# Kernel tuning notes

Hardware: AMD Instinct MI355X
Metric: run time of the kernel (lower is better)

## Reference

```python
import jax, jax.numpy as jnp
import numpy as np

T, D, F, E, K = 2048, 512, 2048, 8, 2


def setup_inputs() -> dict:
    key = jax.random.key(0)
    ks = jax.random.split(key, 5)
    scaled = lambda k, shape, fan: jax.random.normal(k, shape, jnp.float32) * (fan ** -0.5)
    x = jax.random.normal(ks[0], (T, D), jnp.float32)
    Wg = scaled(ks[1], (D, E), D)          # gate: Linear(D -> E), no bias
    W1 = scaled(ks[2], (E, D, F), D)       # per-expert up proj
    W3 = scaled(ks[3], (E, D, F), D)       # per-expert gate proj (SwiGLU)
    W2 = scaled(ks[4], (E, F, D), F)       # per-expert down proj
    return {"x": x, "Wg": Wg, "W1": W1, "W2": W2, "W3": W3}


def reference(x, Wg, W1, W2, W3):
    # gate logits + top-k routing (topk over raw logits, softmax over the k picked logits,
    # computed in float32 then cast back -- matches the torch source)
    logits = x @ Wg                                   # [T, E]
    topw, sel = jax.lax.top_k(logits, K)              # [T, K] each
    weights = jax.nn.softmax(topw.astype(jnp.float32), axis=-1).astype(x.dtype)
    out = jnp.zeros_like(x)
    # NOTE: the source uses `output[batch_idx] = ...` (assignment, not +=), so later
    # experts OVERWRITE earlier ones for tokens routed to multiple experts.
    # We replicate that exactly with sequential jnp.where overwrites.
    for i in range(E):
        hit = sel == i                                # [T, K]
        mask = hit.any(axis=-1)                       # [T] tokens routed to expert i
        w_i = jnp.sum(jnp.where(hit, weights, 0.0), axis=-1)  # [T] routing weight
        h = jax.nn.silu(x @ W1[i]) * (x @ W3[i])      # [T, F] SwiGLU
        y = h @ W2[i]                                 # [T, D]
        out = jnp.where(mask[:, None], w_i[:, None] * y, out)
    return out
```

## Files before the change

kernel.cpp:

```cpp
#include <hip/hip_runtime.h>
#include <hip/hip_bf16.h>
#include <math.h>

typedef __attribute__((ext_vector_type(8))) short short8;
typedef __attribute__((ext_vector_type(4))) float f32x4;

#define T_TOK 2048
#define D_DIM 512
#define F_DIM 2048
#define E_NUM 8
#define MAXT1 40

__device__ __forceinline__ unsigned short f2bf(float f) {
  union { float f; unsigned u; } c; c.f = f;
  unsigned u = c.u;
  return (unsigned short)((u + 0x7fffu + ((u >> 16) & 1u)) >> 16);
}

__device__ __forceinline__ void gld16(const void* g, void* l) {
  __builtin_amdgcn_global_load_lds((const __attribute__((address_space(1))) int*)g,
                                   (__attribute__((address_space(3))) int*)l, 16, 0, 0);
}

__global__ __launch_bounds__(256) void k_route(const float* __restrict__ xin,
                                               const float* __restrict__ Wg,
                                               int* __restrict__ jbuf,
                                               float* __restrict__ wbuf,
                                               unsigned short* __restrict__ xb) {
  int gid = blockIdx.x * 256 + threadIdx.x;
  int t = gid >> 5, seg = gid & 31;
  const float* xp = xin + (size_t)t * D_DIM + seg * 16;
  unsigned short* xo = xb + (size_t)t * D_DIM + seg * 16;
  float acc[8];
#pragma unroll
  for (int e = 0; e < 8; ++e) acc[e] = 0.f;
#pragma unroll
  for (int i = 0; i < 4; ++i) {
    float4 v = *(const float4*)(xp + i * 4);
    ushort4 o;
    o.x = f2bf(v.x); o.y = f2bf(v.y); o.z = f2bf(v.z); o.w = f2bf(v.w);
    *(ushort4*)(xo + i * 4) = o;
    const float* xs = (const float*)&v;
#pragma unroll
    for (int q = 0; q < 4; ++q) {
      int d = seg * 16 + i * 4 + q;
      const float4* wr = (const float4*)(Wg + (size_t)d * 8);
      float4 w0 = wr[0], w1 = wr[1];
      acc[0] += xs[q] * w0.x; acc[1] += xs[q] * w0.y;
      acc[2] += xs[q] * w0.z; acc[3] += xs[q] * w0.w;
      acc[4] += xs[q] * w1.x; acc[5] += xs[q] * w1.y;
      acc[6] += xs[q] * w1.z; acc[7] += xs[q] * w1.w;
    }
  }
#pragma unroll
  for (int off = 1; off < 32; off <<= 1)
#pragma unroll
    for (int e = 0; e < 8; ++e) acc[e] += __shfl_xor(acc[e], off);
  if (seg == 0) {
    float l0 = -1e30f, l1 = -1e30f; int i0 = 0, i1 = 0;
#pragma unroll
    for (int e = 0; e < 8; ++e) {
      float l = acc[e];
      if (l > l0) { l1 = l0; i1 = i0; l0 = l; i0 = e; }
      else if (l > l1) { l1 = l; i1 = e; }
    }
    int j; float w;
    if (i0 > i1) { j = i0; w = 1.f / (1.f + expf(l1 - l0)); }
    else         { j = i1; w = 1.f / (1.f + expf(l0 - l1)); }
    jbuf[t] = j; wbuf[t] = w;
  }
}

__global__ __launch_bounds__(256) void k_prep2(const float* __restrict__ W1,
                                               const float* __restrict__ W3,
                                               unsigned short* __restrict__ w1f,
                                               unsigned short* __restrict__ w3f,
                                               const int* __restrict__ jbuf,
                                               int* __restrict__ cntp,
                                               int* __restrict__ basep,
                                               int* __restrict__ list,
                                               int* __restrict__ tl1,
                                               int* __restrict__ ntl) {
  __shared__ float4 tile4[2][64 * 32];
  __shared__ int scnt[8], scur[8];
  int bz = blockIdx.x, tid = threadIdx.x;

  if (bz >= 1024) {
    if (tid < 8) scnt[tid] = 0;
    __syncthreads();
    for (int t = tid; t < T_TOK; t += 256) atomicAdd(&scnt[jbuf[t]], 1);
    __syncthreads();
    if (tid == 0) {
      int run = 0;
      for (int e = 0; e < 8; ++e) {
        cntp[e] = scnt[e]; basep[e] = run; scur[e] = run;
        run += scnt[e];
      }
      int n1 = 0, bb = 0;
      for (int e = 0; e < 8; ++e) {
        for (int m = 0; m < scnt[e]; m += 64) tl1[n1++] = (e << 16) | (bb + m);
        bb += scnt[e];
      }
      ntl[0] = n1;
    }
    __syncthreads();
    for (int t = tid; t < T_TOK; t += 256) {
      int j = jbuf[t];
      int p = atomicAdd(&scur[j], 1);
      list[p] = t;
    }
    return;
  }

  int z = bz >> 6, rem = bz & 63;
  const int K = 512, N = 2048;
  int n0 = (rem & 15) * 128, k0 = (rem >> 4) * 128;
  size_t zsz = (size_t)(K / 32) * (N / 16) * 512;
  const float* in; unsigned short* out;
  if (z < 8) { in = W1 + (size_t)z * K * N;       out = w1f + (size_t)z * zsz; }
  else       { in = W3 + (size_t)(z - 8) * K * N; out = w3f + (size_t)(z - 8) * zsz; }

  int lr = tid >> 5, lc = tid & 31;
  int wv = tid >> 6, l = tid & 63;
  int n4l = (l & 15) >> 2, nr = l & 3, kg = (l >> 4) * 8;

  auto loadT = [&](int buf, int kb0) {
#pragma unroll
    for (int it = 0; it < 8; ++it) {
      int row = it * 8 + lr;
      float4 v = *(const float4*)(in + (size_t)(kb0 + row) * N + n0 + lc * 4);
      tile4[buf][row * 32 + ((lc + (row >> 3) * 4) & 31)] = v;
    }
  };
  auto storeT = [&](int buf, int kb0) {
    const float* tf = (const float*)&tile4[buf][0];
#pragma unroll
    for (int q = 0; q < 4; ++q) {
      int fid = wv * 4 + q;
      int nb = fid >> 1, kb = fid & 1;
      int n4 = nb * 4 + n4l;
      short8 o;
#pragma unroll
      for (int j = 0; j < 8; ++j) {
        int k = kb * 32 + kg + j;
        int slot = k * 32 + ((n4 + (k >> 3) * 4) & 31);
        o[j] = (short)f2bf(tf[slot * 4 + nr]);
      }
      unsigned short* op = out + (((size_t)(n0 / 16 + nb) * (K / 32)) + (kb0 / 32 + kb)) * 512 + l * 8;
      *(short8*)op = o;
    }
  };

  loadT(0, k0);
  __syncthreads();
  loadT(1, k0 + 64);
  storeT(0, k0);
  __syncthreads();
  storeT(1, k0 + 64);
}

__global__ __launch_bounds__(256, 2) void k_ffn1w2(const unsigned short* __restrict__ xb,
                                                   const unsigned short* __restrict__ w1f,
                                                   const unsigned short* __restrict__ w3f,
                                                   const float* __restrict__ W2,
                                                   unsigned short* __restrict__ w2f,
                                                   const int* __restrict__ cntp,
                                                   const int* __restrict__ basep,
                                                   const int* __restrict__ list,
                                                   const int* __restrict__ tl1,
                                                   const int* __restrict__ ntl,
                                                   unsigned short* __restrict__ hbuf) {
  __shared__ __align__(16) unsigned short sA[64 * 512];
  int tid = threadIdx.x, wv = tid >> 6, l = tid & 63;

  if (blockIdx.x >= 640) {
    int idx = blockIdx.x - 640;
    int z = idx >> 6, rem = idx & 63;
    const int K = 2048, N = 512;
    int n0 = (rem & 3) * 128, k0 = (rem >> 2) * 128;
    size_t zsz = (size_t)(K / 32) * (N / 16) * 512;
    const float* in = W2 + (size_t)z * K * N;
    unsigned short* out = w2f + (size_t)z * zsz;
    float4* tile4 = (float4*)sA;

    int lr = tid >> 5, lc = tid & 31;
    int n4l = (l & 15) >> 2, nr = l & 3, kg = (l >> 4) * 8;

    auto loadT = [&](int buf, int kb0) {
#pragma unroll
      for (int it = 0; it < 8; ++it) {
        int row = it * 8 + lr;
        float4 v = *(const float4*)(in + (size_t)(kb0 + row) * N + n0 + lc * 4);
        tile4[buf * 2048 + row * 32 + ((lc + (row >> 3) * 4) & 31)] = v;
      }
    };
    auto storeT = [&](int buf, int kb0) {
      const float* tf = (const float*)&tile4[buf * 2048];
#pragma unroll
      for (int q = 0; q < 4; ++q) {
        int fid = wv * 4 + q;
        int nb = fid >> 1, kb = fid & 1;
        int n4 = nb * 4 + n4l;
        short8 o;
#pragma unroll
        for (int j = 0; j < 8; ++j) {
          int k = kb * 32 + kg + j;
          int slot = k * 32 + ((n4 + (k >> 3) * 4) & 31);
          o[j] = (short)f2bf(tf[slot * 4 + nr]);
        }
        unsigned short* op = out + (((size_t)(n0 / 16 + nb) * (K / 32)) + (kb0 / 32 + kb)) * 512 + l * 8;
        *(short8*)op = o;
      }
    };

    loadT(0, k0);
    __syncthreads();
    loadT(1, k0 + 64);
    storeT(0, k0);
    __syncthreads();
    storeT(1, k0 + 64);
    return;
  }

  int L = blockIdx.x;
  int b = (L & 7) * 80 + (L >> 3);
  int x = b % 40, y = b / 40;
  if (x >= ntl[0]) return;
  int pk = tl1[x];
  int e = pk >> 16, g0 = pk & 0xffff;
  int lim = basep[e] + cntp[e];
  int wr = wv >> 1, wc = wv & 1;

#pragma unroll
  for (int it = 0; it < 16; ++it) {
    int row = wv * 16 + it;
    int gr = g0 + row; if (gr >= lim) gr = lim - 1;
    int tok = list[gr];
    int slot = (l & 56) | ((l & 7) ^ (row & 7));
    gld16(xb + (size_t)tok * D_DIM + slot * 8, sA + row * 512);
  }

  const unsigned short* w1b = w1f + ((size_t)(e * 128 + y * 8 + wc) * 16) * 512 + l * 8;
  const unsigned short* w3b = w3f + ((size_t)(e * 128 + y * 8 + wc) * 16) * 512 + l * 8;

  short8 P1[8], P3[8], Q1[8], Q3[8];
  auto loadS = [&](short8* r1, short8* r3, int s) {
    int g = s >> 1, h = s & 1;
    const unsigned short* p1 = w1b + ((size_t)(g * 32 + h * 8)) * 512;
    const unsigned short* p3 = w3b + ((size_t)(g * 32 + h * 8)) * 512;
#pragma unroll
    for (int q = 0; q < 8; ++q) {
      r1[q] = *(const short8*)(p1 + (size_t)q * 512);
      r3[q] = *(const short8*)(p3 + (size_t)q * 512);
    }
  };

  f32x4 au[2], av[2];
  auto halfC = [&](const short8* r1, const short8* r3, int h) {
#pragma unroll
    for (int q = 0; q < 8; ++q) {
      int kf = h * 8 + q;
      short8 a[2];
#pragma unroll
      for (int i = 0; i < 2; ++i) {
        int r = wr * 32 + i * 16 + (l & 15);
        int slot = kf * 4 + (l >> 4);
        int swz = (slot & 56) | ((slot & 7) ^ (r & 7));
        a[i] = *(const short8*)(sA + r * 512 + swz * 8);
      }
#pragma unroll
      for (int i = 0; i < 2; ++i) {
        au[i] = __builtin_amdgcn_mfma_f32_16x16x32_bf16(a[i], r1[q], au[i], 0, 0, 0);
        av[i] = __builtin_amdgcn_mfma_f32_16x16x32_bf16(a[i], r3[q], av[i], 0, 0, 0);
      }
    }
  };

  loadS(P1, P3, 0);
  __syncthreads();

  int cloc = l & 15, rb = (l >> 4) * 4;
#pragma unroll
  for (int gp = 0; gp < 4; ++gp) {
#pragma unroll
    for (int i = 0; i < 2; ++i) {
      au[i] = (f32x4){0.f, 0.f, 0.f, 0.f};
      av[i] = (f32x4){0.f, 0.f, 0.f, 0.f};
    }
    loadS(Q1, Q3, gp * 2 + 1);
    halfC(P1, P3, 0);
    if (gp < 3) loadS(P1, P3, gp * 2 + 2);
    halfC(Q1, Q3, 1);
    int col = (y * 4 + gp) * 32 + wc * 16 + cloc;
#pragma unroll
    for (int i = 0; i < 2; ++i)
#pragma unroll
      for (int r = 0; r < 4; ++r) {
        int gr = g0 + wr * 32 + i * 16 + rb + r;
        if (gr < lim) {
          float uu = au[i][r], vv = av[i][r];
          float hh = (uu / (1.f + expf(-uu))) * vv;
          hbuf[(size_t)gr * F_DIM + col] = f2bf(hh);
        }
      }
  }
}

__global__ __launch_bounds__(256, 3) void k_ffn2(const unsigned short* __restrict__ hbuf,
                                                 const unsigned short* __restrict__ w2f,
                                                 const int* __restrict__ cntp,
                                                 const int* __restrict__ basep,
                                                 const int* __restrict__ list,
                                                 const int* __restrict__ tl1,
                                                 const int* __restrict__ ntl,
                                                 const float* __restrict__ wbuf,
                                                 float* __restrict__ out) {
  int L = blockIdx.x;
  int c = L & 7, q = L >> 3;
  int x = c * 5 + (q % 5);
  int nt = q / 5;
  if (x >= ntl[0]) return;
  int pk = tl1[x];
  int e = pk >> 16, g0 = pk & 0xffff;
  int lim = basep[e] + cntp[e];
  __shared__ unsigned short sA[2 * 8192];
  int tid = threadIdx.x, wv = tid >> 6, l = tid & 63;
  int wr = wv >> 1, wc = wv & 1;

  auto stage = [&](int buf, int ck) {
#pragma unroll
    for (int it = 0; it < 4; ++it) {
      int row0 = it * 16 + wv * 4;
      int row = row0 + (l >> 4);
      int gr = g0 + row; if (gr > T_TOK - 1) gr = T_TOK - 1;
      int sl = (l & 8) | ((l & 7) ^ (row & 7));
      gld16(hbuf + (size_t)gr * F_DIM + ck * 128 + sl * 8, sA + buf * 8192 + row0 * 128);
    }
  };

  const unsigned short* b2p = w2f + ((size_t)(e * 32 + nt * 2 + wc) * 64) * 512 + l * 8;

  short8 Ba[4], Bb[4];
  auto loadB = [&](short8* B, int ck) {
#pragma unroll
    for (int kk = 0; kk < 4; ++kk)
      B[kk] = *(const short8*)(b2p + (size_t)(ck * 4 + kk) * 512);
  };

  f32x4 acc[2];
  acc[0] = (f32x4){0.f, 0.f, 0.f, 0.f};
  acc[1] = (f32x4){0.f, 0.f, 0.f, 0.f};

  auto compute = [&](const short8* B, int cur) {
#pragma unroll
    for (int kk = 0; kk < 4; ++kk) {
      short8 a[2];
#pragma unroll
      for (int i = 0; i < 2; ++i) {
        int r = wr * 32 + i * 16 + (l & 15);
        int slot = kk * 4 + (l >> 4);
        int swz = (slot & 8) | ((slot & 7) ^ (r & 7));
        a[i] = *(const short8*)(sA + cur * 8192 + r * 128 + swz * 8);
      }
      acc[0] = __builtin_amdgcn_mfma_f32_16x16x32_bf16(a[0], B[kk], acc[0], 0, 0, 0);
      acc[1] = __builtin_amdgcn_mfma_f32_16x16x32_bf16(a[1], B[kk], acc[1], 0, 0, 0);
    }
  };

  stage(0, 0);
  loadB(Ba, 0);
  __syncthreads();
  int cur = 0;
  for (int ck = 0; ck < 16; ck += 2) {
    stage(cur ^ 1, ck + 1);
    loadB(Bb, ck + 1);
    compute(Ba, cur);
    __syncthreads();
    cur ^= 1;
    if (ck + 2 < 16) {
      stage(cur ^ 1, ck + 2);
      loadB(Ba, ck + 2);
    }
    compute(Bb, cur);
    __syncthreads();
    cur ^= 1;
  }

  int cloc = l & 15, rb = (l >> 4) * 4;
#pragma unroll
  for (int i = 0; i < 2; ++i)
#pragma unroll
    for (int r = 0; r < 4; ++r) {
      int gr = g0 + wr * 32 + i * 16 + rb + r;
      if (gr < lim) {
        int tok = list[gr];
        out[(size_t)tok * D_DIM + nt * 32 + wc * 16 + cloc] = wbuf[tok] * acc[i][r];
      }
    }
}

extern "C" void kernel_launch(void* const* d_in, const int* in_sizes, int n_in,
                              void* d_out, int out_size, void* d_ws, size_t ws_size,
                              hipStream_t stream) {
  const float* x  = (const float*)d_in[0];
  const float* Wg = (const float*)d_in[1];
  const float* W1 = (const float*)d_in[2];
  const float* W2 = (const float*)d_in[3];
  const float* W3 = (const float*)d_in[4];
  float* out = (float*)d_out;
  char* ws = (char*)d_ws;

  int*            jbuf  = (int*)(ws + 0);
  float*          wbuf  = (float*)(ws + 8192);
  int*            cntp  = (int*)(ws + 16384);
  int*            basep = (int*)(ws + 16448);
  int*            list  = (int*)(ws + 16640);
  int*            tl1   = (int*)(ws + 24832);
  int*            ntl   = (int*)(ws + 25600);
  unsigned short* xb    = (unsigned short*)(ws + 32768);
  unsigned short* w1f   = (unsigned short*)(ws + 32768 + 2097152);
  unsigned short* w3f   = (unsigned short*)(ws + 32768 + 2097152 + 16777216);
  unsigned short* w2f   = (unsigned short*)(ws + 32768 + 2097152 + 2 * 16777216);
  unsigned short* hbuf  = (unsigned short*)(ws + 32768 + 2097152 + 3 * 16777216);

  k_route<<<dim3(256), dim3(256), 0, stream>>>(x, Wg, jbuf, wbuf, xb);
  k_prep2<<<dim3(1025), dim3(256), 0, stream>>>(W1, W3, w1f, w3f, jbuf, cntp, basep, list, tl1, ntl);
  k_ffn1w2<<<dim3(1152), dim3(256), 0, stream>>>(xb, w1f, w3f, W2, w2f, cntp, basep, list, tl1, ntl, hbuf);
  k_ffn2<<<dim3(640), dim3(256), 0, stream>>>(hbuf, w2f, cntp, basep, list, tl1, ntl, wbuf, out);
}
```

Before: 80.19 us.

## Shrink FFN1 column tile to 64 per block and double the block count

Each FFN1 block now computes 64 rows by 64 F-columns instead of 64 by 128. The four waves split the columns, and each wave covers all 64 rows with four MFMA accumulator tiles. This doubles the number of FFN1 blocks (the grid goes from 1152 to 1792), so parallelism is higher and per-block latency is shorter. In exchange, each 64x512 token tile is staged into LDS twice as often, and every block still pays the full x-gather cost for half as much compute.

```diff
diff --git a/kernel.cpp b/kernel.cpp
--- a/kernel.cpp
+++ b/kernel.cpp
@@ -173,8 +173,8 @@
   __shared__ __align__(16) unsigned short sA[64 * 512];
   int tid = threadIdx.x, wv = tid >> 6, l = tid & 63;
 
-  if (blockIdx.x >= 640) {
-    int idx = blockIdx.x - 640;
+  if (blockIdx.x >= 1280) {
+    int idx = blockIdx.x - 1280;
     int z = idx >> 6, rem = idx & 63;
     const int K = 2048, N = 512;
     int n0 = (rem & 3) * 128, k0 = (rem >> 2) * 128;
@@ -223,13 +223,12 @@
   }
 
   int L = blockIdx.x;
-  int b = (L & 7) * 80 + (L >> 3);
+  int b = (L & 7) * 160 + (L >> 3);
   int x = b % 40, y = b / 40;
   if (x >= ntl[0]) return;
   int pk = tl1[x];
   int e = pk >> 16, g0 = pk & 0xffff;
   int lim = basep[e] + cntp[e];
-  int wr = wv >> 1, wc = wv & 1;
 
 #pragma unroll
   for (int it = 0; it < 16; ++it) {
@@ -240,36 +239,39 @@
     gld16(xb + (size_t)tok * D_DIM + slot * 8, sA + row * 512);
   }
 
-  const unsigned short* w1b = w1f + ((size_t)(e * 128 + y * 8 + wc) * 16) * 512 + l * 8;
-  const unsigned short* w3b = w3f + ((size_t)(e * 128 + y * 8 + wc) * 16) * 512 + l * 8;
-
-  short8 P1[8], P3[8], Q1[8], Q3[8];
+  const unsigned short* w1b = w1f + ((size_t)(e * 128 + y * 4 + wv) * 16) * 512 + l * 8;
+  const unsigned short* w3b = w3f + ((size_t)(e * 128 + y * 4 + wv) * 16) * 512 + l * 8;
+
+  short8 P1[4], P3[4], Q1[4], Q3[4];
   auto loadS = [&](short8* r1, short8* r3, int s) {
-    int g = s >> 1, h = s & 1;
-    const unsigned short* p1 = w1b + ((size_t)(g * 32 + h * 8)) * 512;
-    const unsigned short* p3 = w3b + ((size_t)(g * 32 + h * 8)) * 512;
-#pragma unroll
-    for (int q = 0; q < 8; ++q) {
-      r1[q] = *(const short8*)(p1 + (size_t)q * 512);
-      r3[q] = *(const short8*)(p3 + (size_t)q * 512);
-    }
-  };
-
-  f32x4 au[2], av[2];
-  auto halfC = [&](const short8* r1, const short8* r3, int h) {
-#pragma unroll
-    for (int q = 0; q < 8; ++q) {
-      int kf = h * 8 + q;
-      short8 a[2];
-#pragma unroll
-      for (int i = 0; i < 2; ++i) {
-        int r = wr * 32 + i * 16 + (l & 15);
+#pragma unroll
+    for (int q = 0; q < 4; ++q) {
+      r1[q] = *(const short8*)(w1b + (size_t)(s * 4 + q) * 512);
+      r3[q] = *(const short8*)(w3b + (size_t)(s * 4 + q) * 512);
+    }
+  };
+
+  f32x4 au[4], av[4];
+#pragma unroll
+  for (int i = 0; i < 4; ++i) {
+    au[i] = (f32x4){0.f, 0.f, 0.f, 0.f};
+    av[i] = (f32x4){0.f, 0.f, 0.f, 0.f};
+  }
+
+  auto quartC = [&](const short8* r1, const short8* r3, int s) {
+#pragma unroll
+    for (int q = 0; q < 4; ++q) {
+      int kf = s * 4 + q;
+      short8 a[4];
+#pragma unroll
+      for (int i = 0; i < 4; ++i) {
+        int r = i * 16 + (l & 15);
         int slot = kf * 4 + (l >> 4);
         int swz = (slot & 56) | ((slot & 7) ^ (r & 7));
         a[i] = *(const short8*)(sA + r * 512 + swz * 8);
       }
 #pragma unroll
-      for (int i = 0; i < 2; ++i) {
+      for (int i = 0; i < 4; ++i) {
         au[i] = __builtin_amdgcn_mfma_f32_16x16x32_bf16(a[i], r1[q], au[i], 0, 0, 0);
         av[i] = __builtin_amdgcn_mfma_f32_16x16x32_bf16(a[i], r3[q], av[i], 0, 0, 0);
       }
@@ -278,32 +280,27 @@
 
   loadS(P1, P3, 0);
   __syncthreads();
+  loadS(Q1, Q3, 1);
+  quartC(P1, P3, 0);
+  loadS(P1, P3, 2);
+  quartC(Q1, Q3, 1);
+  loadS(Q1, Q3, 3);
+  quartC(P1, P3, 2);
+  quartC(Q1, Q3, 3);
 
   int cloc = l & 15, rb = (l >> 4) * 4;
-#pragma unroll
-  for (int gp = 0; gp < 4; ++gp) {
-#pragma unroll
-    for (int i = 0; i < 2; ++i) {
-      au[i] = (f32x4){0.f, 0.f, 0.f, 0.f};
-      av[i] = (f32x4){0.f, 0.f, 0.f, 0.f};
-    }
-    loadS(Q1, Q3, gp * 2 + 1);
-    halfC(P1, P3, 0);
-    if (gp < 3) loadS(P1, P3, gp * 2 + 2);
-    halfC(Q1, Q3, 1);
-    int col = (y * 4 + gp) * 32 + wc * 16 + cloc;
-#pragma unroll
-    for (int i = 0; i < 2; ++i)
-#pragma unroll
-      for (int r = 0; r < 4; ++r) {
-        int gr = g0 + wr * 32 + i * 16 + rb + r;
-        if (gr < lim) {
-          float uu = au[i][r], vv = av[i][r];
-          float hh = (uu / (1.f + expf(-uu))) * vv;
-          hbuf[(size_t)gr * F_DIM + col] = f2bf(hh);
-        }
-      }
-  }
+  int col = y * 64 + wv * 16 + cloc;
+#pragma unroll
+  for (int i = 0; i < 4; ++i)
+#pragma unroll
+    for (int r = 0; r < 4; ++r) {
+      int gr = g0 + i * 16 + rb + r;
+      if (gr < lim) {
+        float uu = au[i][r], vv = av[i][r];
+        float hh = (uu / (1.f + expf(-uu))) * vv;
+        hbuf[(size_t)gr * F_DIM + col] = f2bf(hh);
+      }
+    }
 }
 
 __global__ __launch_bounds__(256, 3) void k_ffn2(const unsigned short* __restrict__ hbuf,
@@ -425,6 +422,6 @@
 
   k_route<<<dim3(256), dim3(256), 0, stream>>>(x, Wg, jbuf, wbuf, xb);
   k_prep2<<<dim3(1025), dim3(256), 0, stream>>>(W1, W3, w1f, w3f, jbuf, cntp, basep, list, tl1, ntl);
-  k_ffn1w2<<<dim3(1152), dim3(256), 0, stream>>>(xb, w1f, w3f, W2, w2f, cntp, basep, list, tl1, ntl, hbuf);
+  k_ffn1w2<<<dim3(1792), dim3(256), 0, stream>>>(xb, w1f, w3f, W2, w2f, cntp, basep, list, tl1, ntl, hbuf);
   k_ffn2<<<dim3(640), dim3(256), 0, stream>>>(hbuf, w2f, cntp, basep, list, tl1, ntl, wbuf, out);
 }
```

New measurement: 76.33 us. -4.8%, faster.
